# Performance work log

Measured on AMD Instinct MI355X. Metric: run time of the kernel, lower is better.

The kernel has to match this reference:

```python
import jax, jax.numpy as jnp
import numpy as np

NBINS = 51
BIN_WIDTH = 2.0 / (NBINS - 1)
BS, D = 1024, 128
N_CLASSES = 32


def setup_inputs() -> dict:
    key = jax.random.key(0)
    kx, kl = jax.random.split(key)
    x = jax.random.normal(kx, (BS, D), dtype=jnp.float32)
    x = x / jnp.linalg.norm(x, axis=1, keepdims=True)  # similarities in [-1, 1]
    labels = jax.random.randint(kl, (BS,), 0, N_CLASSES, dtype=jnp.int64)
    return {"x": x, "labels": labels}


def reference(x, labels):
    # Pairwise similarities of upper-triangular (i < j) pairs.
    sim = x @ x.T                                   # [bs, bs]
    bs = x.shape[0]
    iu, ju = jnp.triu_indices(bs, k=1)              # n_pairs indices
    s = sim[iu, ju]                                 # [n_pairs]
    pos = labels[iu] == labels[ju]                  # [n_pairs] bool

    # Soft (linear) binning: pair with sim s assigned bin value v = floor((s+1)/bw)*bw - 1
    # contributes (v+bw-s)/bw to bin b and (s-v)/bw to bin b+1 (triangular kernel),
    # exactly matching the original indsa/indsb masking scheme.
    b = jnp.floor((s + 1.0) / BIN_WIDTH).astype(jnp.int32)  # bin index in [0, nbins-1]
    v = b.astype(s.dtype) * BIN_WIDTH - 1.0                  # assigned bin value
    w_lo = (v + BIN_WIDTH - s) / BIN_WIDTH                   # weight for bin b
    w_hi = (s - v) / BIN_WIDTH                               # weight for bin b+1
    b_hi = jnp.clip(b + 1, 0, NBINS - 1)                     # w_hi == 0 when clipped

    def hist(mask):
        m = mask.astype(s.dtype)
        h = jnp.zeros((NBINS,), s.dtype)
        h = h.at[b].add(w_lo * m)
        h = h.at[b_hi].add(w_hi * m)
        return h / m.sum()

    hist_pos = hist(pos)
    hist_neg = hist(~pos)

    # CDF of positive histogram, then histogram loss.
    hist_pos_cdf = jnp.cumsum(hist_pos)
    return jnp.sum(hist_neg * hist_pos_cdf)
```

## Files before the change

### kernel.cpp

```cpp
#include <hip/hip_runtime.h>

#define NBINS 51
#define NT    32
#define TILE  32
#define DV4   32
#define NBLK  (NT * (NT + 1) / 2)
#define NCOPY 16
#define HSTR  103
#define NH    (2 * NBINS)
#define PSTR  128

__global__ __launch_bounds__(256) void pair_hist_kernel(
    const float* __restrict__ x,
    const int*   __restrict__ labels,
    float*       __restrict__ gpart)
{
    __shared__ float4 As[TILE][DV4];
    __shared__ float4 Bs[TILE][DV4];
    __shared__ int    la[TILE], lb[TILE];
    __shared__ float  shist[NCOPY * HSTR];

    int rem = blockIdx.x;
    int bi = 0;
    while (rem >= NT - bi) { rem -= NT - bi; ++bi; }
    const int bj = bi + rem;

    const int t = threadIdx.x;
    for (int k = t; k < NCOPY * HSTR; k += 256) shist[k] = 0.0f;

    const float4* xv = (const float4*)x;
    #pragma unroll
    for (int k = 0; k < 4; ++k) {
        int e = t + 256 * k;
        int r = e >> 5;
        int c = e & 31;
        int sw = c ^ ((r >> 1) & 7);
        As[r][sw] = xv[(bi * TILE + r) * DV4 + c];
        Bs[r][sw] = xv[(bj * TILE + r) * DV4 + c];
    }
    if (t < TILE) {
        la[t] = labels[bi * TILE + t];
        lb[t] = labels[bj * TILE + t];
    }
    __syncthreads();

    const int tx = t & 15;
    const int ty = t >> 4;
    const int i0 = ty * 2, j0 = tx * 2;
    const int kA = ty & 7;
    const int kB = tx & 7;

    float acc00 = 0.f, acc01 = 0.f, acc10 = 0.f, acc11 = 0.f;
    #pragma unroll 4
    for (int d4 = 0; d4 < DV4; ++d4) {
        float4 a0 = As[i0    ][d4 ^ kA];
        float4 a1 = As[i0 + 1][d4 ^ kA];
        float4 b0 = Bs[j0    ][d4 ^ kB];
        float4 b1 = Bs[j0 + 1][d4 ^ kB];
        acc00 += a0.x*b0.x + a0.y*b0.y + a0.z*b0.z + a0.w*b0.w;
        acc01 += a0.x*b1.x + a0.y*b1.y + a0.z*b1.z + a0.w*b1.w;
        acc10 += a1.x*b0.x + a1.y*b0.y + a1.z*b0.z + a1.w*b0.w;
        acc11 += a1.x*b1.x + a1.y*b1.y + a1.z*b1.z + a1.w*b1.w;
    }

    const float BW = 2.0f / (NBINS - 1);
    float accs[2][2] = {{acc00, acc01}, {acc10, acc11}};
    float* myh = &shist[(t & (NCOPY - 1)) * HSTR];

    #pragma unroll
    for (int r = 0; r < 2; ++r) {
        #pragma unroll
        for (int c = 0; c < 2; ++c) {
            int gi = bi * TILE + i0 + r;
            int gj = bj * TILE + j0 + c;
            if (gi < gj) {
                float s = accs[r][c];
                int b = (int)floorf((s + 1.0f) / BW);
                b = min(max(b, 0), NBINS - 1);
                float v = (float)b * BW - 1.0f;
                float wlo = (v + BW - s) / BW;
                float whi = (s - v) / BW;
                int bh = min(b + 1, NBINS - 1);
                int base = (la[i0 + r] == lb[j0 + c]) ? 0 : NBINS;
                unsafeAtomicAdd(&myh[base + b],  wlo);
                unsafeAtomicAdd(&myh[base + bh], whi);
            }
        }
    }

    __syncthreads();
    if (t < PSTR) {
        float s = 0.f;
        if (t < NH) {
            #pragma unroll
            for (int c = 0; c < NCOPY; ++c) s += shist[c * HSTR + t];
        }
        gpart[blockIdx.x * PSTR + t] = s;
    }
}

__global__ __launch_bounds__(1024) void finalize_kernel(
    const float* __restrict__ gpart,
    float*       __restrict__ out)
{
    __shared__ float red[32][PSTR];
    __shared__ float tot[PSTR];

    const int t = threadIdx.x;
    const int p = t >> 5;
    const int c = t & 31;

    const float4* g4 = (const float4*)gpart;

    float4 acc = make_float4(0.f, 0.f, 0.f, 0.f);
    #pragma unroll
    for (int k = 0; k < 16; ++k) {
        float4 v = g4[(p + (k << 5)) * 32 + c];
        acc.x += v.x; acc.y += v.y; acc.z += v.z; acc.w += v.w;
    }
    if (p < 16) {
        float4 v = g4[(p + 512) * 32 + c];
        acc.x += v.x; acc.y += v.y; acc.z += v.z; acc.w += v.w;
    }
    *(float4*)&red[p][c * 4] = acc;
    __syncthreads();

    if (t < PSTR) {
        float s = 0.f;
        #pragma unroll
        for (int q = 0; q < 32; ++q) s += red[q][t];
        tot[t] = s;
    }
    __syncthreads();

    if (t < 64) {
        float hp = (t < NBINS) ? tot[t]         : 0.0f;
        float hn = (t < NBINS) ? tot[NBINS + t] : 0.0f;

        float sp = hp, sn = hn;
        #pragma unroll
        for (int off = 32; off > 0; off >>= 1) {
            sp += __shfl_xor(sp, off, 64);
            sn += __shfl_xor(sn, off, 64);
        }

        float cdf = hp;
        #pragma unroll
        for (int off = 1; off < 64; off <<= 1) {
            float v = __shfl_up(cdf, off, 64);
            if (t >= off) cdf += v;
        }

        float contrib = hn * cdf;
        #pragma unroll
        for (int off = 32; off > 0; off >>= 1)
            contrib += __shfl_xor(contrib, off, 64);

        if (t == 0) out[0] = contrib / (sp * sn);
    }
}

extern "C" void kernel_launch(void* const* d_in, const int* in_sizes, int n_in,
                              void* d_out, int out_size, void* d_ws, size_t ws_size,
                              hipStream_t stream)
{
    const float* x      = (const float*)d_in[0];
    const int*   labels = (const int*)d_in[1];
    float*       gpart  = (float*)d_ws;

    pair_hist_kernel<<<NBLK, 256, 0, stream>>>(x, labels, gpart);
    finalize_kernel<<<1, 1024, 0, stream>>>(gpart, (float*)d_out);
}
```

Measured before the change: 72.55 us.

## Fuse finalize into histogram kernel via last-block atomic counter

Merges the two launches into one kernel. Each block writes its partial histogram to a device-global buffer, then bumps an atomic counter, and the last block to arrive does the final reduction, CDF and loss with 256 threads instead of 1024. This removes the second launch and its gap, but the final reduction is now serialized on one block with fewer threads. The counter is reset at the end so later calls work.

Measured after the change: 77.49 us. 1.07x slower.

```diff
diff --git a/kernel.cpp b/kernel.cpp
--- a/kernel.cpp
+++ b/kernel.cpp
@@ -10,15 +10,19 @@
 #define NH    (2 * NBINS)
 #define PSTR  128
 
-__global__ __launch_bounds__(256) void pair_hist_kernel(
+__device__ float g_part[NBLK][PSTR];
+__device__ int   g_counter = 0;
+
+__global__ __launch_bounds__(256) void fused_pair_hist_kernel(
     const float* __restrict__ x,
     const int*   __restrict__ labels,
-    float*       __restrict__ gpart)
+    float*       __restrict__ out)
 {
     __shared__ float4 As[TILE][DV4];
     __shared__ float4 Bs[TILE][DV4];
     __shared__ int    la[TILE], lb[TILE];
     __shared__ float  shist[NCOPY * HSTR];
+    __shared__ int    s_last;
 
     int rem = blockIdx.x;
     int bi = 0;
@@ -95,40 +99,39 @@
             #pragma unroll
             for (int c = 0; c < NCOPY; ++c) s += shist[c * HSTR + t];
         }
-        gpart[blockIdx.x * PSTR + t] = s;
+        g_part[blockIdx.x][t] = s;
     }
-}
+    __syncthreads();
 
-__global__ __launch_bounds__(1024) void finalize_kernel(
-    const float* __restrict__ gpart,
-    float*       __restrict__ out)
-{
-    __shared__ float red[32][PSTR];
-    __shared__ float tot[PSTR];
+    if (t == 0) {
+        __threadfence();
+        s_last = (atomicAdd(&g_counter, 1) == NBLK - 1);
+    }
+    __syncthreads();
+    if (!s_last) return;
 
-    const int t = threadIdx.x;
-    const int p = t >> 5;
-    const int c = t & 31;
+    __threadfence();
 
-    const float4* g4 = (const float4*)gpart;
+    float (*red)[PSTR] = (float (*)[PSTR])As;
+    float* tot = (float*)Bs;
+
+    const int c4 = t & 31;
+    const int p  = t >> 5;
+    const float4* g4 = (const float4*)&g_part[0][0];
 
     float4 acc = make_float4(0.f, 0.f, 0.f, 0.f);
-    #pragma unroll
-    for (int k = 0; k < 16; ++k) {
-        float4 v = g4[(p + (k << 5)) * 32 + c];
+    #pragma unroll 11
+    for (int r = p; r < NBLK; r += 8) {
+        float4 v = g4[r * 32 + c4];
         acc.x += v.x; acc.y += v.y; acc.z += v.z; acc.w += v.w;
     }
-    if (p < 16) {
-        float4 v = g4[(p + 512) * 32 + c];
-        acc.x += v.x; acc.y += v.y; acc.z += v.z; acc.w += v.w;
-    }
-    *(float4*)&red[p][c * 4] = acc;
+    *(float4*)&red[p][c4 * 4] = acc;
     __syncthreads();
 
     if (t < PSTR) {
         float s = 0.f;
         #pragma unroll
-        for (int q = 0; q < 32; ++q) s += red[q][t];
+        for (int q = 0; q < 8; ++q) s += red[q][t];
         tot[t] = s;
     }
     __syncthreads();
@@ -158,6 +161,8 @@
 
         if (t == 0) out[0] = contrib / (sp * sn);
     }
+
+    if (t == 0) g_counter = 0;
 }
 
 extern "C" void kernel_launch(void* const* d_in, const int* in_sizes, int n_in,
@@ -166,8 +171,6 @@
 {
     const float* x      = (const float*)d_in[0];
     const int*   labels = (const int*)d_in[1];
-    float*       gpart  = (float*)d_ws;
 
-    pair_hist_kernel<<<NBLK, 256, 0, stream>>>(x, labels, gpart);
-    finalize_kernel<<<1, 1024, 0, stream>>>(gpart, (float*)d_out);
+    fused_pair_hist_kernel<<<NBLK, 256, 0, stream>>>(x, labels, (float*)d_out);
 }
```
